# Performance work log

Measured on AMD Instinct MI355X. Metric: run time of the kernel, lower is better.

## Reference

```python
import jax, jax.numpy as jnp
import numpy as np

TEMPERATURE = 8.0  # sqrt(d_k=64)
NEG_FILL = -1000.0


def setup_inputs() -> dict:
    key = jax.random.key(0)
    k1, k2, k3, k4 = jax.random.split(key, 4)
    B, Lq, Lk, D = 16, 2048, 2048, 64
    q = jax.random.normal(k1, (B, Lq, D), dtype=jnp.float32)
    k = jax.random.normal(k2, (B, Lk, D), dtype=jnp.float32)
    v = jax.random.normal(k3, (B, Lk, D), dtype=jnp.float32)
    pad_mask = jax.random.randint(k4, (B, Lk), 0, 2).astype(bool)
    return {"q": q, "k": k, "v": v, "pad_mask": pad_mask}


def reference(q, k, v, pad_mask):
    # scores: [B, Lq, Lk]
    attn = jnp.einsum('bqd,bkd->bqk', q, k) / TEMPERATURE
    # mask padded keys (broadcast over query dim, like pad_mask.unsqueeze(1))
    attn = jnp.where(pad_mask[:, None, :], NEG_FILL, attn)
    attn = jax.nn.softmax(attn, axis=-1)
    # dropout is identity in eval / p=0
    output = jnp.einsum('bqk,bkd->bqd', attn, v)
    return output, attn
```

## Files before the change

### kernel.cpp

```cpp
#include <hip/hip_runtime.h>
#include <hip/hip_bf16.h>

#define BB 16
#define LL 2048
#define DD 64

typedef __attribute__((ext_vector_type(8))) short short8t;
typedef __attribute__((ext_vector_type(4))) float f32x4;
typedef __attribute__((ext_vector_type(4))) unsigned short ushort4t;

__device__ __forceinline__ unsigned short f2bf(float x) {
  union { float f; unsigned int u; } c; c.f = x;
  unsigned int u = c.u;
  u += 0x7fffu + ((u >> 16) & 1u);
  return (unsigned short)(u >> 16);
}

__device__ __forceinline__ int cvt_pk_bf16(float lo, float hi) {
  int r;
  asm("v_cvt_pk_bf16_f32 %0, %1, %2" : "=v"(r) : "v"(lo), "v"(hi));
  return r;
}

__global__ void cvt_bf16(const float* __restrict__ in, unsigned short* __restrict__ out) {
  int i = (blockIdx.x * 256 + threadIdx.x) * 4;
  float4 v = *(const float4*)(in + i);
  ushort4t o;
  o.x = f2bf(v.x); o.y = f2bf(v.y); o.z = f2bf(v.z); o.w = f2bf(v.w);
  *(ushort4t*)(out + i) = o;
}

__global__ void vtrans(const float* __restrict__ v, unsigned short* __restrict__ vt) {
  __shared__ unsigned short t[64][66];
  int b = blockIdx.x >> 5, j0 = (blockIdx.x & 31) * 64;
  const float* src = v + ((size_t)b * LL + j0) * DD;
#pragma unroll
  for (int i = 0; i < 16; ++i) {
    int lin = i * 256 + threadIdx.x;
    int j = lin >> 6, d = lin & 63;
    t[j][d] = f2bf(src[lin]);
  }
  __syncthreads();
  unsigned short* dst = vt + (size_t)b * DD * LL;
#pragma unroll
  for (int i = 0; i < 16; ++i) {
    int lin = i * 256 + threadIdx.x;
    int d = lin >> 6, j = lin & 63;
    dst[(size_t)d * LL + j0 + j] = t[j][d];
  }
}

__device__ __forceinline__ void async_cp16(const unsigned short* src, unsigned short* dst_lds) {
  __builtin_amdgcn_global_load_lds(
      (const __attribute__((address_space(1))) unsigned int*)src,
      (__attribute__((address_space(3))) unsigned int*)dst_lds, 16, 0, 0);
}

__global__ void __launch_bounds__(256, 2)
attn_main(const unsigned short* __restrict__ Qb, const unsigned short* __restrict__ Kb,
          const unsigned short* __restrict__ VTb, const int* __restrict__ mask,
          float* __restrict__ out, float* __restrict__ attn) {
  __shared__ __align__(16) unsigned short TB[4][8704];
  __shared__ float redF[256];
  __shared__ float rinvF[64];

  const int tid = threadIdx.x;
  const int w = tid >> 6;
  const int l = tid & 63;
  const int l15 = l & 15;
  const int g = l >> 4;

  const int swzb = (blockIdx.x & 7) * 64 + (blockIdx.x >> 3);
  const int b = swzb >> 5;
  const int q0 = (swzb & 31) << 6;

  unsigned short* K0 = &TB[w][0];
  unsigned short* K1 = &TB[w][2048];
  unsigned short* VB = &TB[w][4096];
  float* PW = (float*)&TB[w][6144];

  const unsigned short* Kbb = Kb + (size_t)b * LL * DD;
  const unsigned short* VTbb = VTb + (size_t)b * DD * LL;
  const int* maskb = mask + b * LL;

  auto loadK = [&](int k0, unsigned short* KB) {
    const unsigned short* gs = Kbb + (size_t)k0 * DD;
#pragma unroll
    for (int i2 = 0; i2 < 4; ++i2) {
      int row = i2 * 8 + (l >> 3);
      int ce = (l & 7) * 8;
      async_cp16(gs + row * 64 + (ce ^ ((row & 3) << 4)), KB + i2 * 512);
    }
  };
  auto loadV = [&](int k0) {
    const unsigned short* gs = VTbb + k0;
#pragma unroll
    for (int i2 = 0; i2 < 4; ++i2) {
      int row = i2 * 16 + (l >> 2);
      int ce = (l & 3) * 8;
      async_cp16(gs + (size_t)row * LL + (ce ^ ((row & 1) << 4)), VB + i2 * 512);
    }
  };

  short8t qf[4][2];
  {
    const unsigned short* qbase = Qb + ((size_t)b * LL + q0 + l15) * DD + 8 * g;
#pragma unroll
    for (int mi = 0; mi < 4; ++mi)
#pragma unroll
      for (int h = 0; h < 2; ++h)
        qf[mi][h] = *(const short8t*)(qbase + mi * 16 * DD + 32 * h);
  }

  float ls[4] = {0.f, 0.f, 0.f, 0.f};

  auto stepA = [&](int t, int tn, unsigned short* KBc, unsigned short* KBn,
                   const int4& m0c, const int4& m1c, int4& m0n, int4& m1n) {
    asm volatile("s_waitcnt vmcnt(0)" ::: "memory");
    loadK(tn * 32, KBn);
    m0n = *(const int4*)(maskb + tn * 32 + 4 * g);
    m1n = *(const int4*)(maskb + tn * 32 + 16 + 4 * g);

    short8t kf[2][2];
#pragma unroll
    for (int ni = 0; ni < 2; ++ni)
#pragma unroll
      for (int h = 0; h < 2; ++h) {
        int row = 16 * ni + l15;
        int col = (32 * h + 8 * g) ^ ((l15 & 3) << 4);
        kf[ni][h] = *(const short8t*)(KBc + row * 64 + col);
      }

    f32x4 sacc[4][2] = {};
    __builtin_amdgcn_s_setprio(1);
#pragma unroll
    for (int mi = 0; mi < 4; ++mi)
#pragma unroll
      for (int ni = 0; ni < 2; ++ni)
#pragma unroll
        for (int h = 0; h < 2; ++h)
          sacc[mi][ni] = __builtin_amdgcn_mfma_f32_16x16x32_bf16(kf[ni][h], qf[mi][h], sacc[mi][ni], 0, 0, 0);
    __builtin_amdgcn_s_setprio(0);
#pragma unroll
    for (int mi = 0; mi < 4; ++mi)
#pragma unroll
      for (int ni = 0; ni < 2; ++ni) {
        const int* mk = ni ? (const int*)&m1c : (const int*)&m0c;
#pragma unroll
        for (int r = 0; r < 4; ++r)
          ls[mi] += mk[r] ? 0.f : __expf(sacc[mi][ni][r] * 0.125f);
      }
  };

  {
    loadK(w * 32, K0);
    int4 a0 = *(const int4*)(maskb + w * 32 + 4 * g);
    int4 a1 = *(const int4*)(maskb + w * 32 + 16 + 4 * g);
    int4 b0, b1;
    for (int j = 0; j < 8; ++j) {
      int t = w + 8 * j;
      stepA(t, t + 4, K0, K1, a0, a1, b0, b1);
      int t2 = t + 4;
      int tn = (j == 7) ? w : (t2 + 4);
      stepA(t2, tn, K1, K0, b0, b1, a0, a1);
    }
  }

  {
#pragma unroll
    for (int mi = 0; mi < 4; ++mi) {
      float s = ls[mi];
      s += __shfl_xor(s, 16);
      s += __shfl_xor(s, 32);
      ls[mi] = s;
    }
    if (l < 16) {
#pragma unroll
      for (int mi = 0; mi < 4; ++mi) redF[w * 64 + 16 * mi + l] = ls[mi];
    }
  }
  __syncthreads();
  if (tid < 64)
    rinvF[tid] = 1.0f / (redF[tid] + redF[64 + tid] + redF[128 + tid] + redF[192 + tid]);
  __syncthreads();

  float rinv_[4];
#pragma unroll
  for (int mi = 0; mi < 4; ++mi) rinv_[mi] = rinvF[16 * mi + l15];

  f32x4 oacc[4][4] = {};
  const size_t arow = (size_t)b * LL + q0;
  auto stepB = [&](int t, int tn, const unsigned short* KBc, unsigned short* KBn,
                   const int4& m0c, const int4& m1c, int4& m0n, int4& m1n) {
    asm volatile("s_waitcnt vmcnt(8)" ::: "memory");
    const int k0 = t * 32;

    short8t kf[2][2], vf[4];
#pragma unroll
    for (int ni = 0; ni < 2; ++ni)
#pragma unroll
      for (int h = 0; h < 2; ++h) {
        int row = 16 * ni + l15;
        int col = (32 * h + 8 * g) ^ ((l15 & 3) << 4);
        kf[ni][h] = *(const short8t*)(KBc + row * 64 + col);
      }
#pragma unroll
    for (int ni = 0; ni < 4; ++ni)
      vf[ni] = *(const short8t*)(VB + (16 * ni + l15) * 32 + ((8 * g) ^ ((l & 1) << 4)));
    asm volatile("s_waitcnt lgkmcnt(0)" ::: "memory");
    __builtin_amdgcn_sched_barrier(0);

    loadK(tn * 32, KBn);
    m0n = *(const int4*)(maskb + tn * 32 + 4 * g);
    m1n = *(const int4*)(maskb + tn * 32 + 16 + 4 * g);
    loadV(tn * 32);

    f32x4 sacc[4][2] = {};
    __builtin_amdgcn_s_setprio(1);
#pragma unroll
    for (int mi = 0; mi < 4; ++mi)
#pragma unroll
      for (int ni = 0; ni < 2; ++ni)
#pragma unroll
        for (int h = 0; h < 2; ++h)
          sacc[mi][ni] = __builtin_amdgcn_mfma_f32_16x16x32_bf16(kf[ni][h], qf[mi][h], sacc[mi][ni], 0, 0, 0);
    __builtin_amdgcn_s_setprio(0);

#pragma unroll
    for (int mi = 0; mi < 4; ++mi) {
      f32x4 pv0, pv1;
#pragma unroll
      for (int r = 0; r < 4; ++r) {
        pv0[r] = ((const int*)&m0c)[r] ? 0.f : __expf(sacc[mi][0][r] * 0.125f) * rinv_[mi];
        pv1[r] = ((const int*)&m1c)[r] ? 0.f : __expf(sacc[mi][1][r] * 0.125f) * rinv_[mi];
      }
      float* dst = attn + (arow + 16 * mi + l15) * LL + k0 + 4 * g;
      *(f32x4*)(dst) = pv0;
      *(f32x4*)(dst + 16) = pv1;
      int2 pa, pb;
      pa.x = cvt_pk_bf16(pv0[0], pv0[1]);
      pa.y = cvt_pk_bf16(pv0[2], pv0[3]);
      pb.x = cvt_pk_bf16(pv1[0], pv1[1]);
      pb.y = cvt_pk_bf16(pv1[2], pv1[3]);
      float* pwm = PW + mi * 320 + l15 * 20;
      *(int2*)(pwm + 2 * g) = pa;
      *(int2*)(pwm + 8 + 2 * g) = pb;
    }
    asm volatile("s_waitcnt lgkmcnt(0)" ::: "memory");
    __builtin_amdgcn_sched_barrier(0);

    short8t pfr[4];
#pragma unroll
    for (int mi = 0; mi < 4; ++mi)
      pfr[mi] = *(const short8t*)(PW + mi * 320 + l15 * 20 + 4 * g);

    __builtin_amdgcn_s_setprio(1);
#pragma unroll
    for (int mi = 0; mi < 4; ++mi)
#pragma unroll
      for (int ni = 0; ni < 4; ++ni)
        oacc[mi][ni] = __builtin_amdgcn_mfma_f32_16x16x32_bf16(pfr[mi], vf[ni], oacc[mi][ni], 0, 0, 0);
    __builtin_amdgcn_s_setprio(0);
  };

  {
    loadK(w * 32, K0);
    int4 a0 = *(const int4*)(maskb + w * 32 + 4 * g);
    int4 a1 = *(const int4*)(maskb + w * 32 + 16 + 4 * g);
    loadV(w * 32);
    asm volatile("s_waitcnt vmcnt(0)" ::: "memory");
    int4 b0, b1;
    for (int j = 0; j < 8; ++j) {
      int t = w + 8 * j;
      stepB(t, t + 4, K0, K1, a0, a1, b0, b1);
      int t2 = t + 4;
      int tn = (j == 7) ? w : (t2 + 4);
      stepB(t2, tn, K1, K0, b0, b1, a0, a1);
    }
  }

  asm volatile("s_waitcnt vmcnt(0)" ::: "memory");

  __syncthreads();
  float* OB = (float*)&TB[0][0];
  if (w) {
#pragma unroll
    for (int mi = 0; mi < 4; ++mi)
#pragma unroll
      for (int ni = 0; ni < 4; ++ni)
#pragma unroll
        for (int r = 0; r < 4; ++r)
          OB[(w - 1) * 4096 + (16 * mi + 4 * g + r) * 64 + 16 * ni + l15] = oacc[mi][ni][r];
  }
  __syncthreads();
  if (w == 0) {
#pragma unroll
    for (int mi = 0; mi < 4; ++mi)
#pragma unroll
      for (int ni = 0; ni < 4; ++ni)
#pragma unroll
        for (int r = 0; r < 4; ++r) {
          int pos = (16 * mi + 4 * g + r) * 64 + 16 * ni + l15;
          OB[12288 + pos] = oacc[mi][ni][r] + OB[pos] + OB[4096 + pos] + OB[8192 + pos];
        }
  }
  __syncthreads();
#pragma unroll
  for (int it = 0; it < 4; ++it) {
    int lin = it * 256 + tid;
    int row = lin >> 4;
    int c4 = (lin & 15) * 4;
    float4 o4 = *(const float4*)(OB + 12288 + row * 64 + c4);
    *(float4*)(out + ((size_t)(b * LL + q0 + row)) * DD + c4) = o4;
  }
}

extern "C" void kernel_launch(void* const* d_in, const int* in_sizes, int n_in,
                              void* d_out, int out_size, void* d_ws, size_t ws_size,
                              hipStream_t stream) {
  const float* q = (const float*)d_in[0];
  const float* k = (const float*)d_in[1];
  const float* v = (const float*)d_in[2];
  const int* pm = (const int*)d_in[3];

  float* out = (float*)d_out;
  float* attn = out + (size_t)BB * LL * DD;

  unsigned short* Qb = (unsigned short*)d_ws;
  unsigned short* Kb = Qb + (size_t)BB * LL * DD;
  unsigned short* VT = Kb + (size_t)BB * LL * DD;

  cvt_bf16<<<2048, 256, 0, stream>>>(q, Qb);
  cvt_bf16<<<2048, 256, 0, stream>>>(k, Kb);
  vtrans<<<512, 256, 0, stream>>>(v, VT);
  attn_main<<<512, 256, 0, stream>>>(Qb, Kb, VT, pm, out, attn);
}
```

Baseline: 91.55 us.

## Halve query tile, fuse prep kernels, fold softmax scale into Q for exp2

```diff
diff --git a/kernel.cpp b/kernel.cpp
--- a/kernel.cpp
+++ b/kernel.cpp
@@ -4,6 +4,7 @@
 #define BB 16
 #define LL 2048
 #define DD 64
+#define QSCALE 0.1803368801111602f
 
 typedef __attribute__((ext_vector_type(8))) short short8t;
 typedef __attribute__((ext_vector_type(4))) float f32x4;
@@ -22,31 +23,41 @@
   return r;
 }
 
-__global__ void cvt_bf16(const float* __restrict__ in, unsigned short* __restrict__ out) {
-  int i = (blockIdx.x * 256 + threadIdx.x) * 4;
-  float4 v = *(const float4*)(in + i);
-  ushort4t o;
-  o.x = f2bf(v.x); o.y = f2bf(v.y); o.z = f2bf(v.z); o.w = f2bf(v.w);
-  *(ushort4t*)(out + i) = o;
-}
-
-__global__ void vtrans(const float* __restrict__ v, unsigned short* __restrict__ vt) {
+__global__ void prep(const float* __restrict__ q, const float* __restrict__ k,
+                     const float* __restrict__ v,
+                     unsigned short* __restrict__ Qb, unsigned short* __restrict__ Kb,
+                     unsigned short* __restrict__ VT) {
   __shared__ unsigned short t[64][66];
-  int b = blockIdx.x >> 5, j0 = (blockIdx.x & 31) * 64;
-  const float* src = v + ((size_t)b * LL + j0) * DD;
-#pragma unroll
-  for (int i = 0; i < 16; ++i) {
-    int lin = i * 256 + threadIdx.x;
-    int j = lin >> 6, d = lin & 63;
-    t[j][d] = f2bf(src[lin]);
-  }
-  __syncthreads();
-  unsigned short* dst = vt + (size_t)b * DD * LL;
-#pragma unroll
-  for (int i = 0; i < 16; ++i) {
-    int lin = i * 256 + threadIdx.x;
-    int d = lin >> 6, j = lin & 63;
-    dst[(size_t)d * LL + j0 + j] = t[j][d];
+  int bid = blockIdx.x;
+  if (bid < 4096) {
+    bool isQ = bid < 2048;
+    const float* in = isQ ? q : k;
+    unsigned short* outp = isQ ? Qb : Kb;
+    float sc = isQ ? QSCALE : 1.0f;
+    int i = (bid & 2047) * 1024 + threadIdx.x * 4;
+    float4 v4 = *(const float4*)(in + i);
+    ushort4t o;
+    o.x = f2bf(v4.x * sc); o.y = f2bf(v4.y * sc);
+    o.z = f2bf(v4.z * sc); o.w = f2bf(v4.w * sc);
+    *(ushort4t*)(outp + i) = o;
+  } else {
+    int vb = bid - 4096;
+    int b = vb >> 5, j0 = (vb & 31) * 64;
+    const float* src = v + ((size_t)b * LL + j0) * DD;
+#pragma unroll
+    for (int i = 0; i < 16; ++i) {
+      int lin = i * 256 + threadIdx.x;
+      int j = lin >> 6, d = lin & 63;
+      t[j][d] = f2bf(src[lin]);
+    }
+    __syncthreads();
+    unsigned short* dst = VT + (size_t)b * DD * LL;
+#pragma unroll
+    for (int i = 0; i < 16; ++i) {
+      int lin = i * 256 + threadIdx.x;
+      int d = lin >> 6, j = lin & 63;
+      dst[(size_t)d * LL + j0 + j] = t[j][d];
+    }
   }
 }
 
@@ -56,13 +67,13 @@
       (__attribute__((address_space(3))) unsigned int*)dst_lds, 16, 0, 0);
 }
 
-__global__ void __launch_bounds__(256, 2)
+__global__ void __launch_bounds__(256, 3)
 attn_main(const unsigned short* __restrict__ Qb, const unsigned short* __restrict__ Kb,
           const unsigned short* __restrict__ VTb, const int* __restrict__ mask,
           float* __restrict__ out, float* __restrict__ attn) {
-  __shared__ __align__(16) unsigned short TB[4][8704];
-  __shared__ float redF[256];
-  __shared__ float rinvF[64];
+  __shared__ __align__(16) unsigned short TB[4][6144];
+  __shared__ float redF[128];
+  __shared__ float rinvF[32];
 
   const int tid = threadIdx.x;
   const int w = tid >> 6;
@@ -70,14 +81,13 @@
   const int l15 = l & 15;
   const int g = l >> 4;
 
-  const int swzb = (blockIdx.x & 7) * 64 + (blockIdx.x >> 3);
-  const int b = swzb >> 5;
-  const int q0 = (swzb & 31) << 6;
+  const int swzb = (blockIdx.x & 7) * 128 + (blockIdx.x >> 3);
+  const int b = swzb >> 6;
+  const int q0 = (swzb & 63) << 5;
 
   unsigned short* K0 = &TB[w][0];
   unsigned short* K1 = &TB[w][2048];
   unsigned short* VB = &TB[w][4096];
-  float* PW = (float*)&TB[w][6144];
 
   const unsigned short* Kbb = Kb + (size_t)b * LL * DD;
   const unsigned short* VTbb = VTb + (size_t)b * DD * LL;
@@ -102,17 +112,17 @@
     }
   };
 
-  short8t qf[4][2];
+  short8t qf[2][2];
   {
     const unsigned short* qbase = Qb + ((size_t)b * LL + q0 + l15) * DD + 8 * g;
 #pragma unroll
-    for (int mi = 0; mi < 4; ++mi)
+    for (int mi = 0; mi < 2; ++mi)
 #pragma unroll
       for (int h = 0; h < 2; ++h)
         qf[mi][h] = *(const short8t*)(qbase + mi * 16 * DD + 32 * h);
   }
 
-  float ls[4] = {0.f, 0.f, 0.f, 0.f};
+  float ls[2] = {0.f, 0.f};
 
   auto stepA = [&](int t, int tn, unsigned short* KBc, unsigned short* KBn,
                    const int4& m0c, const int4& m1c, int4& m0n, int4& m1n) {
@@ -131,10 +141,10 @@
         kf[ni][h] = *(const short8t*)(KBc + row * 64 + col);
       }
 
-    f32x4 sacc[4][2] = {};
+    f32x4 sacc[2][2] = {};
     __builtin_amdgcn_s_setprio(1);
 #pragma unroll
-    for (int mi = 0; mi < 4; ++mi)
+    for (int mi = 0; mi < 2; ++mi)
 #pragma unroll
       for (int ni = 0; ni < 2; ++ni)
 #pragma unroll
@@ -142,13 +152,13 @@
           sacc[mi][ni] = __builtin_amdgcn_mfma_f32_16x16x32_bf16(kf[ni][h], qf[mi][h], sacc[mi][ni], 0, 0, 0);
     __builtin_amdgcn_s_setprio(0);
 #pragma unroll
-    for (int mi = 0; mi < 4; ++mi)
+    for (int mi = 0; mi < 2; ++mi)
 #pragma unroll
       for (int ni = 0; ni < 2; ++ni) {
         const int* mk = ni ? (const int*)&m1c : (const int*)&m0c;
 #pragma unroll
         for (int r = 0; r < 4; ++r)
-          ls[mi] += mk[r] ? 0.f : __expf(sacc[mi][ni][r] * 0.125f);
+          ls[mi] += mk[r] ? 0.f : exp2f(sacc[mi][ni][r]);
       }
   };
 
@@ -168,7 +178,7 @@
 
   {
 #pragma unroll
-    for (int mi = 0; mi < 4; ++mi) {
+    for (int mi = 0; mi < 2; ++mi) {
       float s = ls[mi];
       s += __shfl_xor(s, 16);
       s += __shfl_xor(s, 32);
@@ -176,23 +186,23 @@
     }
     if (l < 16) {
 #pragma unroll
-      for (int mi = 0; mi < 4; ++mi) redF[w * 64 + 16 * mi + l] = ls[mi];
+      for (int mi = 0; mi < 2; ++mi) redF[w * 32 + 16 * mi + l] = ls[mi];
     }
   }
   __syncthreads();
-  if (tid < 64)
-    rinvF[tid] = 1.0f / (redF[tid] + redF[64 + tid] + redF[128 + tid] + redF[192 + tid]);
+  if (tid < 32)
+    rinvF[tid] = 1.0f / (redF[tid] + redF[32 + tid] + redF[64 + tid] + redF[96 + tid]);
   __syncthreads();
 
-  float rinv_[4];
-#pragma unroll
-  for (int mi = 0; mi < 4; ++mi) rinv_[mi] = rinvF[16 * mi + l15];
-
-  f32x4 oacc[4][4] = {};
+  float rinv_[2];
+#pragma unroll
+  for (int mi = 0; mi < 2; ++mi) rinv_[mi] = rinvF[16 * mi + l15];
+
+  f32x4 oacc[2][4] = {};
   const size_t arow = (size_t)b * LL + q0;
-  auto stepB = [&](int t, int tn, const unsigned short* KBc, unsigned short* KBn,
+  auto stepB = [&](int t, int tn, unsigned short* KBc, unsigned short* KBn,
                    const int4& m0c, const int4& m1c, int4& m0n, int4& m1n) {
-    asm volatile("s_waitcnt vmcnt(8)" ::: "memory");
+    asm volatile("s_waitcnt vmcnt(4)" ::: "memory");
     const int k0 = t * 32;
 
     short8t kf[2][2], vf[4];
@@ -215,10 +225,10 @@
     m1n = *(const int4*)(maskb + tn * 32 + 16 + 4 * g);
     loadV(tn * 32);
 
-    f32x4 sacc[4][2] = {};
+    f32x4 sacc[2][2] = {};
     __builtin_amdgcn_s_setprio(1);
 #pragma unroll
-    for (int mi = 0; mi < 4; ++mi)
+    for (int mi = 0; mi < 2; ++mi)
 #pragma unroll
       for (int ni = 0; ni < 2; ++ni)
 #pragma unroll
@@ -226,13 +236,15 @@
           sacc[mi][ni] = __builtin_amdgcn_mfma_f32_16x16x32_bf16(kf[ni][h], qf[mi][h], sacc[mi][ni], 0, 0, 0);
     __builtin_amdgcn_s_setprio(0);
 
-#pragma unroll
-    for (int mi = 0; mi < 4; ++mi) {
+    float* PWp = (float*)KBc;
+    const int xorv = (l15 & 3) << 2;
+#pragma unroll
+    for (int mi = 0; mi < 2; ++mi) {
       f32x4 pv0, pv1;
 #pragma unroll
       for (int r = 0; r < 4; ++r) {
-        pv0[r] = ((const int*)&m0c)[r] ? 0.f : __expf(sacc[mi][0][r] * 0.125f) * rinv_[mi];
-        pv1[r] = ((const int*)&m1c)[r] ? 0.f : __expf(sacc[mi][1][r] * 0.125f) * rinv_[mi];
+        pv0[r] = ((const int*)&m0c)[r] ? 0.f : exp2f(sacc[mi][0][r]) * rinv_[mi];
+        pv1[r] = ((const int*)&m1c)[r] ? 0.f : exp2f(sacc[mi][1][r]) * rinv_[mi];
       }
       float* dst = attn + (arow + 16 * mi + l15) * LL + k0 + 4 * g;
       *(f32x4*)(dst) = pv0;
@@ -242,21 +254,21 @@
       pa.y = cvt_pk_bf16(pv0[2], pv0[3]);
       pb.x = cvt_pk_bf16(pv1[0], pv1[1]);
       pb.y = cvt_pk_bf16(pv1[2], pv1[3]);
-      float* pwm = PW + mi * 320 + l15 * 20;
-      *(int2*)(pwm + 2 * g) = pa;
-      *(int2*)(pwm + 8 + 2 * g) = pb;
+      float* pwm = PWp + mi * 256 + l15 * 16;
+      *(int2*)(pwm + ((2 * g) ^ xorv)) = pa;
+      *(int2*)(pwm + ((8 + 2 * g) ^ xorv)) = pb;
     }
     asm volatile("s_waitcnt lgkmcnt(0)" ::: "memory");
     __builtin_amdgcn_sched_barrier(0);
 
-    short8t pfr[4];
-#pragma unroll
-    for (int mi = 0; mi < 4; ++mi)
-      pfr[mi] = *(const short8t*)(PW + mi * 320 + l15 * 20 + 4 * g);
+    short8t pfr[2];
+#pragma unroll
+    for (int mi = 0; mi < 2; ++mi)
+      pfr[mi] = *(const short8t*)(PWp + mi * 256 + l15 * 16 + ((4 * g) ^ xorv));
 
     __builtin_amdgcn_s_setprio(1);
 #pragma unroll
-    for (int mi = 0; mi < 4; ++mi)
+    for (int mi = 0; mi < 2; ++mi)
 #pragma unroll
       for (int ni = 0; ni < 4; ++ni)
         oacc[mi][ni] = __builtin_amdgcn_mfma_f32_16x16x32_bf16(pfr[mi], vf[ni], oacc[mi][ni], 0, 0, 0);
@@ -285,33 +297,25 @@
   float* OB = (float*)&TB[0][0];
   if (w) {
 #pragma unroll
-    for (int mi = 0; mi < 4; ++mi)
+    for (int mi = 0; mi < 2; ++mi)
 #pragma unroll
       for (int ni = 0; ni < 4; ++ni)
 #pragma unroll
         for (int r = 0; r < 4; ++r)
-          OB[(w - 1) * 4096 + (16 * mi + 4 * g + r) * 64 + 16 * ni + l15] = oacc[mi][ni][r];
+          OB[(w - 1) * 2048 + (16 * mi + 4 * g + r) * 64 + 16 * ni + l15] = oacc[mi][ni][r];
   }
   __syncthreads();
   if (w == 0) {
 #pragma unroll
-    for (int mi = 0; mi < 4; ++mi)
+    for (int mi = 0; mi < 2; ++mi)
 #pragma unroll
       for (int ni = 0; ni < 4; ++ni)
 #pragma unroll
         for (int r = 0; r < 4; ++r) {
           int pos = (16 * mi + 4 * g + r) * 64 + 16 * ni + l15;
-          OB[12288 + pos] = oacc[mi][ni][r] + OB[pos] + OB[4096 + pos] + OB[8192 + pos];
+          out[(arow + 16 * mi + 4 * g + r) * DD + 16 * ni + l15] =
+              oacc[mi][ni][r] + OB[pos] + OB[2048 + pos] + OB[4096 + pos];
         }
-  }
-  __syncthreads();
-#pragma unroll
-  for (int it = 0; it < 4; ++it) {
-    int lin = it * 256 + tid;
-    int row = lin >> 4;
-    int c4 = (lin & 15) * 4;
-    float4 o4 = *(const float4*)(OB + 12288 + row * 64 + c4);
-    *(float4*)(out + ((size_t)(b * LL + q0 + row)) * DD + c4) = o4;
   }
 }
 
@@ -330,8 +334,6 @@
   unsigned short* Kb = Qb + (size_t)BB * LL * DD;
   unsigned short* VT = Kb + (size_t)BB * LL * DD;
 
-  cvt_bf16<<<2048, 256, 0, stream>>>(q, Qb);
-  cvt_bf16<<<2048, 256, 0, stream>>>(k, Kb);
-  vtrans<<<512, 256, 0, stream>>>(v, VT);
-  attn_main<<<512, 256, 0, stream>>>(Qb, Kb, VT, pm, out, attn);
-}
+  prep<<<4608, 256, 0, stream>>>(q, k, v, Qb, Kb, VT);
+  attn_main<<<1024, 256, 0, stream>>>(Qb, Kb, VT, pm, out, attn);
+}
```

After: 104.6 us. +14.3%, slower.
